# Optimization experiments

Hardware: AMD Instinct MI355X
Metric: run time of the kernel (lower is better)

## Reference

```python
import jax, jax.numpy as jnp
import numpy as np

N = 100_000      # nodes
E = 1_600_000    # edges
F_IN = 256       # num_node_features
H = 128          # hidden_dim
G = 1_000        # graphs in batch


def setup_inputs() -> dict:
    key = jax.random.key(0)
    ks = jax.random.split(key, 12)
    x = jax.random.normal(ks[0], (N, F_IN), jnp.float32)
    edge_index = jax.random.randint(ks[1], (2, E), 0, N)
    batch = jnp.sort(jax.random.randint(ks[2], (N,), 0, G))
    def w(k, shape):
        fan_in = shape[0]
        return jax.random.normal(k, shape, jnp.float32) / np.sqrt(fan_in)
    return {
        "x": x,
        "edge_index": edge_index,
        "batch": batch,
        "W1": w(ks[3], (F_IN, H)), "b1": jnp.zeros((H,), jnp.float32),
        "W2": w(ks[4], (H, H)),    "b2": jnp.zeros((H,), jnp.float32),
        "W3": w(ks[5], (H, H)),    "b3": jnp.zeros((H,), jnp.float32),
        "fw1": w(ks[6], (H, 32)),  "fb1": jnp.zeros((32,), jnp.float32),
        "fw2": w(ks[7], (32, 2)),  "fb2": jnp.zeros((2,), jnp.float32),
    }


def reference(x, edge_index, batch, W1, b1, W2, b2, W3, b3, fw1, fb1, fw2, fb2):
    # GCN normalization with self-loops (PyG GCNConv defaults)
    loop = jnp.arange(N)
    src = jnp.concatenate([edge_index[0], loop])  # [E+N]
    dst = jnp.concatenate([edge_index[1], loop])
    deg = jax.ops.segment_sum(jnp.ones(E + N, x.dtype), dst, num_segments=N)
    dis = jnp.where(deg > 0, jax.lax.rsqrt(deg), 0.0)
    norm = (dis[src] * dis[dst])[:, None]  # [E+N, 1]

    def gcn(h, W, b):
        h = h @ W                                    # linear transform first (fewer bytes moved)
        msg = h[src] * norm                          # gather + scale
        return jax.ops.segment_sum(msg, dst, num_segments=N) + b  # scatter-add

    h = jax.nn.relu(gcn(x, W1, b1))   # dropout = identity (eval mode)
    h = jax.nn.relu(gcn(h, W2, b2))
    h = jax.nn.relu(gcn(h, W3, b3))

    # global_mean_pool over graph ids
    sums = jax.ops.segment_sum(h, batch, num_segments=G)          # [G, H]
    cnt = jax.ops.segment_sum(jnp.ones(N, h.dtype), batch, num_segments=G)
    g = sums / jnp.maximum(cnt, 1.0)[:, None]

    g = jax.nn.relu(g @ fw1 + fb1)
    logits = g @ fw2 + fb2
    return jax.nn.log_softmax(logits, axis=1)
```

## Files before the change

kernel.cpp:

```cpp
#include <hip/hip_runtime.h>
#include <hip/hip_bf16.h>
#include <math.h>

#define N_NODES 100000
#define N_EDGES 1600000
#define F_IN 256
#define H_DIM 128
#define N_GRAPHS 1000

#define NB_BUCKETS ((N_NODES + 255) >> 8)
#define BSTRIDE 392
#define A_BLOCKS 256
#define EPB (N_EDGES / A_BLOCKS)

typedef unsigned short bfu;
typedef unsigned char u8;
typedef short short8 __attribute__((ext_vector_type(8)));
typedef float f32x4 __attribute__((ext_vector_type(4)));
typedef float f32x2 __attribute__((ext_vector_type(2)));

__device__ __forceinline__ float b2f(unsigned u) {
    union { unsigned int i; float f; } v;
    v.i = u << 16;
    return v.f;
}
__device__ __forceinline__ bfu f2b(float f) {
    __hip_bfloat16 h = __float2bfloat16(f);
    return *reinterpret_cast<bfu*>(&h);
}
__device__ __forceinline__ unsigned pk4_fp8(float v0, float v1, float v2, float v3) {
    int r = __builtin_amdgcn_cvt_pk_fp8_f32(v0, v1, 0, false);
    r = __builtin_amdgcn_cvt_pk_fp8_f32(v2, v3, r, true);
    return (unsigned)r;
}
__device__ __forceinline__ void acc4_fp8(float* a, unsigned v) {
    f32x2 p;
    p = __builtin_amdgcn_cvt_pk_f32_fp8((int)v, false); a[0] += p.x; a[1] += p.y;
    p = __builtin_amdgcn_cvt_pk_f32_fp8((int)v, true);  a[2] += p.x; a[3] += p.y;
}
__device__ __forceinline__ uint4 fp8x8_to_bf16x8(uint2 v) {
    f32x2 p0 = __builtin_amdgcn_cvt_pk_f32_fp8((int)v.x, false);
    f32x2 p1 = __builtin_amdgcn_cvt_pk_f32_fp8((int)v.x, true);
    f32x2 p2 = __builtin_amdgcn_cvt_pk_f32_fp8((int)v.y, false);
    f32x2 p3 = __builtin_amdgcn_cvt_pk_f32_fp8((int)v.y, true);
    uint4 o;
    o.x = (unsigned)f2b(p0.x) | ((unsigned)f2b(p0.y) << 16);
    o.y = (unsigned)f2b(p1.x) | ((unsigned)f2b(p1.y) << 16);
    o.z = (unsigned)f2b(p2.x) | ((unsigned)f2b(p2.y) << 16);
    o.w = (unsigned)f2b(p3.x) | ((unsigned)f2b(p3.y) << 16);
    return o;
}

__global__ __launch_bounds__(256) void k_hist(const int* __restrict__ dst,
                                              int* __restrict__ cnt_bb) {
    __shared__ int h[BSTRIDE];
    const int t = threadIdx.x;
    for (int i = t; i < BSTRIDE; i += 256) h[i] = 0;
    __syncthreads();
    const int base = blockIdx.x * EPB;
    for (int i = t; i < EPB; i += 256) atomicAdd(&h[dst[base + i] >> 8], 1);
    __syncthreads();
    for (int i = t; i < NB_BUCKETS; i += 256) cnt_bb[blockIdx.x * BSTRIDE + i] = h[i];
}

__global__ __launch_bounds__(256) void k_scan_blocks(int* __restrict__ cnt_bb,
                                                     int* __restrict__ btot) {
    __shared__ int s[256];
    const int t = threadIdx.x;
    const int b = blockIdx.x;
    int v = cnt_bb[t * BSTRIDE + b];
    s[t] = v;
    __syncthreads();
    for (int off = 1; off < 256; off <<= 1) {
        int u = (t >= off) ? s[t - off] : 0;
        __syncthreads();
        s[t] += u;
        __syncthreads();
    }
    cnt_bb[t * BSTRIDE + b] = s[t] - v;
    if (t == 255) btot[b] = s[255];
}

__global__ __launch_bounds__(256) void k_stage(const int* __restrict__ src,
                                               const int* __restrict__ dst,
                                               const int* __restrict__ cnt_bb,
                                               const int* __restrict__ bucket_base,
                                               unsigned* __restrict__ staging) {
    __shared__ int cur[BSTRIDE];
    const int t = threadIdx.x;
    const int blk = blockIdx.x;
    for (int i = t; i < NB_BUCKETS; i += 256)
        cur[i] = bucket_base[i] + cnt_bb[blk * BSTRIDE + i];
    __syncthreads();
    const int base = blk * EPB;
    for (int i = t; i < EPB; i += 256) {
        int d = dst[base + i];
        int s = src[base + i];
        int b = d >> 8;
        int pos = atomicAdd(&cur[b], 1);
        staging[pos] = (unsigned)s | ((unsigned)(d & 255) << 24);
    }
}

__global__ __launch_bounds__(256) void k_bucket(const unsigned* __restrict__ staging,
                                                const int* __restrict__ bucket_base,
                                                int* __restrict__ row_ptr,
                                                float* __restrict__ dis,
                                                int* __restrict__ col) {
    __shared__ int h[256];
    __shared__ int sc[256];
    __shared__ int cur[256];
    const int t = threadIdx.x;
    const int b = blockIdx.x;
    const int s0 = bucket_base[b];
    const int ne = bucket_base[b + 1] - s0;
    h[t] = 0;
    __syncthreads();
    for (int i = t; i < ne; i += 256) atomicAdd(&h[staging[s0 + i] >> 24], 1);
    __syncthreads();
    int myc = h[t];
    sc[t] = myc;
    __syncthreads();
    for (int off = 1; off < 256; off <<= 1) {
        int u = (t >= off) ? sc[t - off] : 0;
        __syncthreads();
        sc[t] += u;
        __syncthreads();
    }
    int excl = sc[t] - myc;
    int node = b * 256 + t;
    if (node <= N_NODES) row_ptr[node] = s0 + excl;
    if (node < N_NODES) dis[node] = rsqrtf((float)(myc + 1));
    cur[t] = s0 + excl;
    __syncthreads();
    for (int i = t; i < ne; i += 256) {
        unsigned u = staging[s0 + i];
        int pos = atomicAdd(&cur[u >> 24], 1);
        col[pos] = (int)(u & 0xFFFFFFu);
    }
}

__device__ __forceinline__ void wpack_one(const float* __restrict__ W,
                                          bfu* __restrict__ Wp, int u) {
    int lane = u & 63;
    int nf = (u >> 6) & 7;
    int ks = u >> 9;
    int k = ks * 32 + (lane >> 4) * 8;
    int n = nf * 16 + (lane & 15);
    bfu o[8];
#pragma unroll
    for (int j = 0; j < 8; ++j) o[j] = f2b(W[(k + j) * 128 + n]);
    uint4 pk;
    pk.x = (unsigned)o[0] | ((unsigned)o[1] << 16);
    pk.y = (unsigned)o[2] | ((unsigned)o[3] << 16);
    pk.z = (unsigned)o[4] | ((unsigned)o[5] << 16);
    pk.w = (unsigned)o[6] | ((unsigned)o[7] << 16);
    *(uint4*)&Wp[u * 8] = pk;
}

__global__ __launch_bounds__(256) void k_misc(const float* __restrict__ W1,
                                              const float* __restrict__ W2,
                                              const float* __restrict__ W3,
                                              bfu* __restrict__ wp1, bfu* __restrict__ wp2,
                                              bfu* __restrict__ wp3,
                                              const int* __restrict__ batch,
                                              int* __restrict__ bounds,
                                              const int* __restrict__ btot,
                                              int* __restrict__ bucket_base) {
    const int b = blockIdx.x, t = threadIdx.x;
    if (b < 16) {
        wpack_one(W1, wp1, b * 256 + t);
    } else if (b < 24) {
        wpack_one(W2, wp2, (b - 16) * 256 + t);
    } else if (b < 32) {
        wpack_one(W3, wp3, (b - 24) * 256 + t);
    } else if (b < 36) {
        int g = (b - 32) * 256 + t;
        if (g <= N_GRAPHS) {
            int lo = 0, hi = N_NODES;
            while (lo < hi) {
                int mid = (lo + hi) >> 1;
                if (batch[mid] < g) lo = mid + 1; else hi = mid;
            }
            bounds[g] = lo;
        }
    } else {
        __shared__ int s[256];
        int g0 = 2 * t, g1 = 2 * t + 1;
        int v0 = (g0 < NB_BUCKETS) ? btot[g0] : 0;
        int v1 = (g1 < NB_BUCKETS) ? btot[g1] : 0;
        int pair = v0 + v1;
        s[t] = pair;
        __syncthreads();
        for (int off = 1; off < 256; off <<= 1) {
            int u = (t >= off) ? s[t - off] : 0;
            __syncthreads();
            s[t] += u;
            __syncthreads();
        }
        int excl = s[t] - pair;
        if (g0 < NB_BUCKETS) bucket_base[g0] = excl;
        if (g1 < NB_BUCKETS) bucket_base[g1] = excl + v0;
        if (t == 0) bucket_base[NB_BUCKETS] = N_EDGES;
    }
}

__global__ __launch_bounds__(256, 2) void k_mm1(const float* __restrict__ A,
                                                const bfu* __restrict__ Wp,
                                                const float* __restrict__ dis,
                                                u8* __restrict__ C8, int M) {
    const int t = threadIdx.x;
    const int w = t >> 6, l = t & 63, l15 = l & 15, lhi = l >> 4;
    const int row = blockIdx.x * 64 + w * 16 + l15;
    const int rowc = row < M ? row : M - 1;
    const float* ap = A + (long)rowc * 256 + lhi * 8;

    float4 buf[4][2];
#pragma unroll
    for (int i = 0; i < 4; ++i) {
        buf[i][0] = *(const float4*)(ap + i * 32);
        buf[i][1] = *(const float4*)(ap + i * 32 + 4);
    }

    f32x4 acc[8];
#pragma unroll
    for (int nf = 0; nf < 8; ++nf) acc[nf] = (f32x4)0.0f;

#pragma unroll
    for (int ks = 0; ks < 8; ++ks) {
        float4 c0 = buf[ks & 3][0];
        float4 c1 = buf[ks & 3][1];
        if (ks + 4 < 8) {
            buf[ks & 3][0] = *(const float4*)(ap + (ks + 4) * 32);
            buf[ks & 3][1] = *(const float4*)(ap + (ks + 4) * 32 + 4);
        }
        unsigned p0 = (unsigned)f2b(c0.x) | ((unsigned)f2b(c0.y) << 16);
        unsigned p1 = (unsigned)f2b(c0.z) | ((unsigned)f2b(c0.w) << 16);
        unsigned p2 = (unsigned)f2b(c1.x) | ((unsigned)f2b(c1.y) << 16);
        unsigned p3 = (unsigned)f2b(c1.z) | ((unsigned)f2b(c1.w) << 16);
        uint4 afu = make_uint4(p0, p1, p2, p3);
        short8 af = *(short8*)&afu;
        const bfu* wp = Wp + ((long)(ks * 8) * 64 + l) * 8;
#pragma unroll
        for (int nf = 0; nf < 8; ++nf) {
            short8 wf = *(const short8*)(wp + (long)nf * 64 * 8);
            acc[nf] = __builtin_amdgcn_mfma_f32_16x16x32_bf16(wf, af, acc[nf], 0, 0, 0);
        }
    }
    if (row < M) {
        float sc = dis[row];
        int nb0 = lhi * 4;
#pragma unroll
        for (int nf = 0; nf < 8; ++nf) {
            unsigned pk = pk4_fp8(acc[nf][0] * sc, acc[nf][1] * sc,
                                  acc[nf][2] * sc, acc[nf][3] * sc);
            *(unsigned*)&C8[(long)row * 128 + nf * 16 + nb0] = pk;
        }
    }
}

template <bool OUT_BF16>
__global__ __launch_bounds__(256) void k_agg8(const int* __restrict__ row_ptr,
                                              const int* __restrict__ col,
                                              const float* __restrict__ dis,
                                              const u8* __restrict__ t8,
                                              const float* __restrict__ b,
                                              bfu* __restrict__ h16,
                                              u8* __restrict__ h8) {
    const int t = threadIdx.x;
    const int node = blockIdx.x * 8 + (t >> 5);
    const int lane = t & 31;
    if (node >= N_NODES) return;
    const int q = lane << 2;

    const u8* tp = t8 + q;
    float a[4] = {0.f, 0.f, 0.f, 0.f};
    acc4_fp8(a, *(const unsigned*)&tp[(long)node * 128]);

    int e = row_ptr[node];
    const int end = row_ptr[node + 1];
    for (; e + 7 < end; e += 8) {
        unsigned v[8];
#pragma unroll
        for (int j = 0; j < 8; ++j) v[j] = *(const unsigned*)&tp[(long)col[e + j] * 128];
#pragma unroll
        for (int j = 0; j < 8; ++j) acc4_fp8(a, v[j]);
    }
    for (; e + 3 < end; e += 4) {
        unsigned v0 = *(const unsigned*)&tp[(long)col[e] * 128];
        unsigned v1 = *(const unsigned*)&tp[(long)col[e + 1] * 128];
        unsigned v2 = *(const unsigned*)&tp[(long)col[e + 2] * 128];
        unsigned v3 = *(const unsigned*)&tp[(long)col[e + 3] * 128];
        acc4_fp8(a, v0); acc4_fp8(a, v1); acc4_fp8(a, v2); acc4_fp8(a, v3);
    }
    for (; e < end; ++e)
        acc4_fp8(a, *(const unsigned*)&tp[(long)col[e] * 128]);

    const float dn = dis[node];
    float4 bb = *(const float4*)&b[q];
    float o0 = fmaxf(a[0] * dn + bb.x, 0.0f);
    float o1 = fmaxf(a[1] * dn + bb.y, 0.0f);
    float o2 = fmaxf(a[2] * dn + bb.z, 0.0f);
    float o3 = fmaxf(a[3] * dn + bb.w, 0.0f);
    if (OUT_BF16) {
        uint2 pk;
        pk.x = (unsigned)f2b(o0) | ((unsigned)f2b(o1) << 16);
        pk.y = (unsigned)f2b(o2) | ((unsigned)f2b(o3) << 16);
        *(uint2*)&h16[(long)node * 128 + q] = pk;
    } else {
        *(unsigned*)&h8[(long)node * 128 + q] = pk4_fp8(o0, o1, o2, o3);
    }
}

__global__ __launch_bounds__(256) void k_mm2(const u8* __restrict__ A8,
                                             const bfu* __restrict__ Wp,
                                             const float* __restrict__ dis,
                                             u8* __restrict__ C8, int M) {
    __shared__ bfu As[2][64 * 40];
    const int t = threadIdx.x;
    const int w = t >> 6;
    const int l = t & 63;
    const int l15 = l & 15;
    const int lhi = l >> 4;
    const int row0 = blockIdx.x * 64;

    f32x4 acc[8];
#pragma unroll
    for (int nf = 0; nf < 8; ++nf) acc[nf] = (f32x4)0.0f;

    uint2 pb = make_uint2(0u, 0u);
    {
        int r = t >> 2, s = t & 3;
        if (row0 + r < M) pb = *(const uint2*)&A8[(long)(row0 + r) * 128 + s * 8];
    }

    int buf = 0;
#pragma unroll
    for (int ks = 0; ks < 4; ++ks) {
        *(uint4*)&As[buf][(t >> 2) * 40 + (t & 3) * 8] = fp8x8_to_bf16x8(pb);
        if (ks + 1 < 4) {
            const int k0n = (ks + 1) * 32;
            int r = t >> 2, s = t & 3;
            pb = make_uint2(0u, 0u);
            if (row0 + r < M) pb = *(const uint2*)&A8[(long)(row0 + r) * 128 + k0n + s * 8];
        }
        __syncthreads();
        short8 af = *(const short8*)&As[buf][(w * 16 + l15) * 40 + lhi * 8];
        const bfu* wp = Wp + ((long)(ks * 8) * 64 + l) * 8;
#pragma unroll
        for (int nf = 0; nf < 8; ++nf) {
            short8 wf = *(const short8*)(wp + (long)nf * 64 * 8);
            acc[nf] = __builtin_amdgcn_mfma_f32_16x16x32_bf16(wf, af, acc[nf], 0, 0, 0);
        }
        if (ks + 1 < 4) __syncthreads();
        buf ^= 1;
    }
    int row = row0 + w * 16 + l15;
    if (row < M) {
        float sc = dis[row];
        int nb0 = lhi * 4;
#pragma unroll
        for (int nf = 0; nf < 8; ++nf) {
            unsigned pko = pk4_fp8(acc[nf][0] * sc, acc[nf][1] * sc,
                                   acc[nf][2] * sc, acc[nf][3] * sc);
            *(unsigned*)&C8[(long)row * 128 + nf * 16 + nb0] = pko;
        }
    }
}

__global__ __launch_bounds__(128) void k_pool_head(const int* __restrict__ bounds,
                                                   const bfu* __restrict__ h,
                                                   const float* __restrict__ fw1, const float* __restrict__ fb1,
                                                   const float* __restrict__ fw2, const float* __restrict__ fb2,
                                                   float* __restrict__ out) {
    const int g = blockIdx.x;
    const int t = threadIdx.x;
    const int s = bounds[g], e = bounds[g + 1];
    float sum = 0.0f;
    int n = s;
    for (; n + 1 < e; n += 2) {
        sum += b2f(h[(long)n * 128 + t]);
        sum += b2f(h[(long)(n + 1) * 128 + t]);
    }
    if (n < e) sum += b2f(h[(long)n * 128 + t]);

    __shared__ float sg[128];
    __shared__ float sh[32];
    float inv = 1.0f / fmaxf((float)(e - s), 1.0f);
    sg[t] = sum * inv;
    __syncthreads();
    if (t < 32) {
        float a = fb1[t];
#pragma unroll 8
        for (int k = 0; k < 128; ++k) a += sg[k] * fw1[k * 32 + t];
        sh[t] = fmaxf(a, 0.0f);
    }
    __syncthreads();
    if (t == 0) {
        float l0 = fb2[0], l1 = fb2[1];
        for (int k = 0; k < 32; ++k) {
            l0 += sh[k] * fw2[k * 2];
            l1 += sh[k] * fw2[k * 2 + 1];
        }
        float m = fmaxf(l0, l1);
        float lse = m + logf(expf(l0 - m) + expf(l1 - m));
        out[g * 2 + 0] = l0 - lse;
        out[g * 2 + 1] = l1 - lse;
    }
}

extern "C" void kernel_launch(void* const* d_in, const int* in_sizes, int n_in,
                              void* d_out, int out_size, void* d_ws, size_t ws_size,
                              hipStream_t stream) {
    const float* x  = (const float*)d_in[0];
    const int* ei   = (const int*)d_in[1];
    const int* batch = (const int*)d_in[2];
    const float* W1 = (const float*)d_in[3];
    const float* b1 = (const float*)d_in[4];
    const float* W2 = (const float*)d_in[5];
    const float* b2 = (const float*)d_in[6];
    const float* W3 = (const float*)d_in[7];
    const float* b3 = (const float*)d_in[8];
    const float* fw1 = (const float*)d_in[9];
    const float* fb1 = (const float*)d_in[10];
    const float* fw2 = (const float*)d_in[11];
    const float* fb2 = (const float*)d_in[12];
    float* out = (float*)d_out;

    const int* src = ei;
    const int* dst = ei + N_EDGES;

    char* ws = (char*)d_ws;
    int*      cnt_bb      = (int*)ws;
    int*      btot        = cnt_bb + A_BLOCKS * BSTRIDE;
    int*      bucket_base = btot + BSTRIDE;
    unsigned* staging     = (unsigned*)(bucket_base + BSTRIDE + 8);
    int*      row_ptr     = (int*)(staging + N_EDGES);
    float*    dis         = (float*)(row_ptr + N_NODES + 4);
    int*      col         = (int*)(dis + N_NODES);
    int*      bounds      = col + N_EDGES;
    bfu*      wpack1      = (bfu*)(bounds + N_GRAPHS + 8);
    bfu*      wpack2      = wpack1 + 32768;
    bfu*      wpack3      = wpack2 + 16384;
    u8*       bufT8       = (u8*)(wpack3 + 16384);
    u8*       bufH8       = bufT8 + (long)N_NODES * 128;
    bfu*      bufH        = (bfu*)(bufH8 + (long)N_NODES * 128);

    k_hist<<<A_BLOCKS, 256, 0, stream>>>(dst, cnt_bb);
    k_scan_blocks<<<NB_BUCKETS, 256, 0, stream>>>(cnt_bb, btot);
    k_misc<<<37, 256, 0, stream>>>(W1, W2, W3, wpack1, wpack2, wpack3, batch, bounds,
                                   btot, bucket_base);
    k_stage<<<A_BLOCKS, 256, 0, stream>>>(src, dst, cnt_bb, bucket_base, staging);
    k_bucket<<<NB_BUCKETS, 256, 0, stream>>>(staging, bucket_base, row_ptr, dis, col);

    const int mm1Grid = (N_NODES + 63) / 64;
    const int mm2Grid = (N_NODES + 63) / 64;
    const int aggGrid = (N_NODES + 7) / 8;

    k_mm1<<<mm1Grid, 256, 0, stream>>>(x, wpack1, dis, bufT8, N_NODES);
    k_agg8<false><<<aggGrid, 256, 0, stream>>>(row_ptr, col, dis, bufT8, b1, nullptr, bufH8);
    k_mm2<<<mm2Grid, 256, 0, stream>>>(bufH8, wpack2, dis, bufT8, N_NODES);
    k_agg8<false><<<aggGrid, 256, 0, stream>>>(row_ptr, col, dis, bufT8, b2, nullptr, bufH8);
    k_mm2<<<mm2Grid, 256, 0, stream>>>(bufH8, wpack3, dis, bufT8, N_NODES);
    k_agg8<true><<<aggGrid, 256, 0, stream>>>(row_ptr, col, dis, bufT8, b3, bufH, nullptr);

    k_pool_head<<<N_GRAPHS, 128, 0, stream>>>(bounds, bufH, fw1, fb1, fw2, fb2, out);
}
```

Measured before the change: 302.2 us.

## Stream mm1 input tiles into LDS via direct global-to-LDS loads with double buffering

The first GEMM kernel no longer loads each lane's A row slices into registers with a four-deep prefetch ring. It now stages 64x32 fp32 tiles into a double-buffered, XOR-swizzled LDS buffer using global_load_lds, then reads the fragments from LDS. This coalesces the global reads and frees registers, and the launch-bounds occupancy hint is dropped. In exchange it adds two block barriers per k-step and an extra pass through LDS.

```diff
diff --git a/kernel.cpp b/kernel.cpp
--- a/kernel.cpp
+++ b/kernel.cpp
@@ -49,6 +49,11 @@
     o.z = (unsigned)f2b(p2.x) | ((unsigned)f2b(p2.y) << 16);
     o.w = (unsigned)f2b(p3.x) | ((unsigned)f2b(p3.y) << 16);
     return o;
+}
+__device__ __forceinline__ void gl_lds16(const void* g, void* lds) {
+    __builtin_amdgcn_global_load_lds(
+        (const __attribute__((address_space(1))) unsigned int*)g,
+        (__attribute__((address_space(3))) unsigned int*)lds, 16, 0, 0);
 }
 
 __global__ __launch_bounds__(256) void k_hist(const int* __restrict__ dst,
@@ -205,39 +210,46 @@
     }
 }
 
-__global__ __launch_bounds__(256, 2) void k_mm1(const float* __restrict__ A,
-                                                const bfu* __restrict__ Wp,
-                                                const float* __restrict__ dis,
-                                                u8* __restrict__ C8, int M) {
+__global__ __launch_bounds__(256) void k_mm1(const float* __restrict__ A,
+                                             const bfu* __restrict__ Wp,
+                                             const float* __restrict__ dis,
+                                             u8* __restrict__ C8, int M) {
+    __shared__ float Xs[2][2048];
     const int t = threadIdx.x;
     const int w = t >> 6, l = t & 63, l15 = l & 15, lhi = l >> 4;
-    const int row = blockIdx.x * 64 + w * 16 + l15;
-    const int rowc = row < M ? row : M - 1;
-    const float* ap = A + (long)rowc * 256 + lhi * 8;
-
-    float4 buf[4][2];
-#pragma unroll
-    for (int i = 0; i < 4; ++i) {
-        buf[i][0] = *(const float4*)(ap + i * 32);
-        buf[i][1] = *(const float4*)(ap + i * 32 + 4);
-    }
+    const int row0 = blockIdx.x * 64;
+
+    const int i0 = w * 64 + l;
+    const int i1 = 256 + w * 64 + l;
+    const int r0 = i0 >> 3, fo0 = ((i0 & 7) ^ (r0 & 7)) * 4;
+    const int r1 = i1 >> 3, fo1 = ((i1 & 7) ^ (r1 & 7)) * 4;
+    const float* g0 = A + (long)((row0 + r0) < M ? (row0 + r0) : 0) * 256 + fo0;
+    const float* g1 = A + (long)((row0 + r1) < M ? (row0 + r1) : 0) * 256 + fo1;
 
     f32x4 acc[8];
 #pragma unroll
     for (int nf = 0; nf < 8; ++nf) acc[nf] = (f32x4)0.0f;
 
+    gl_lds16(g0, &Xs[0][w * 256]);
+    gl_lds16(g1, &Xs[0][1024 + w * 256]);
+
+    int buf = 0;
+    const int rr = w * 16 + l15;
+    const int ca = (lhi * 2) ^ (rr & 7);
+    const int cb = (lhi * 2 + 1) ^ (rr & 7);
 #pragma unroll
     for (int ks = 0; ks < 8; ++ks) {
-        float4 c0 = buf[ks & 3][0];
-        float4 c1 = buf[ks & 3][1];
-        if (ks + 4 < 8) {
-            buf[ks & 3][0] = *(const float4*)(ap + (ks + 4) * 32);
-            buf[ks & 3][1] = *(const float4*)(ap + (ks + 4) * 32 + 4);
-        }
-        unsigned p0 = (unsigned)f2b(c0.x) | ((unsigned)f2b(c0.y) << 16);
-        unsigned p1 = (unsigned)f2b(c0.z) | ((unsigned)f2b(c0.w) << 16);
-        unsigned p2 = (unsigned)f2b(c1.x) | ((unsigned)f2b(c1.y) << 16);
-        unsigned p3 = (unsigned)f2b(c1.z) | ((unsigned)f2b(c1.w) << 16);
+        __syncthreads();
+        if (ks + 1 < 8) {
+            gl_lds16(g0 + (ks + 1) * 32, &Xs[buf ^ 1][w * 256]);
+            gl_lds16(g1 + (ks + 1) * 32, &Xs[buf ^ 1][1024 + w * 256]);
+        }
+        float4 fa = *(const float4*)&Xs[buf][rr * 32 + ca * 4];
+        float4 fb = *(const float4*)&Xs[buf][rr * 32 + cb * 4];
+        unsigned p0 = (unsigned)f2b(fa.x) | ((unsigned)f2b(fa.y) << 16);
+        unsigned p1 = (unsigned)f2b(fa.z) | ((unsigned)f2b(fa.w) << 16);
+        unsigned p2 = (unsigned)f2b(fb.x) | ((unsigned)f2b(fb.y) << 16);
+        unsigned p3 = (unsigned)f2b(fb.z) | ((unsigned)f2b(fb.w) << 16);
         uint4 afu = make_uint4(p0, p1, p2, p3);
         short8 af = *(short8*)&afu;
         const bfu* wp = Wp + ((long)(ks * 8) * 64 + l) * 8;
@@ -246,7 +258,11 @@
             short8 wf = *(const short8*)(wp + (long)nf * 64 * 8);
             acc[nf] = __builtin_amdgcn_mfma_f32_16x16x32_bf16(wf, af, acc[nf], 0, 0, 0);
         }
-    }
+        __syncthreads();
+        buf ^= 1;
+    }
+
+    int row = row0 + rr;
     if (row < M) {
         float sc = dis[row];
         int nb0 = lhi * 4;
```

Result: no change. 298.7 us (-1.1%).
